# Kernel optimization log

Hardware: AMD Instinct MI355X
Metric: run time of the kernel (lower is better)

## Reference

```python
import jax, jax.numpy as jnp
import numpy as np


def setup_inputs() -> dict:
    key = jax.random.key(0)
    k1, k2 = jax.random.split(key)
    B, N, M = 4, 16384, 4096
    src_points = jax.random.normal(k1, (B, N, 3), dtype=jnp.float32)
    target_verts = jax.random.normal(k2, (B, M, 3), dtype=jnp.float32)
    return {"src_points": src_points, "target_verts": target_verts}


def reference(src_points, target_verts):
    # target_faces=None path of ChamferLoss: degenerate one-vertex triangles,
    # so closest-point-on-mesh == nearest target vertex.
    # d2[b,n,m] = ||p_bn - v_bm||^2 via the expansion p2 + v2 - 2 p.v
    p2 = jnp.sum(src_points * src_points, axis=-1)          # (B, N)
    v2 = jnp.sum(target_verts * target_verts, axis=-1)      # (B, M)
    pv = jnp.einsum('bnd,bmd->bnm', src_points, target_verts)  # (B, N, M)
    d2 = p2[:, :, None] + v2[:, None, :] - 2.0 * pv
    d2 = jnp.maximum(d2, 0.0)
    min_d2 = jnp.min(d2, axis=-1)                            # (B, N)
    num_src_per_batch = src_points.shape[1]
    loss = jnp.sum(min_d2, axis=-1) / num_src_per_batch      # (B,)
    return loss
```

## Files before the change

kernel.cpp:

```cpp
#include <hip/hip_runtime.h>
#include <float.h>


typedef __bf16 bf16x8 __attribute__((ext_vector_type(8)));
typedef float  f32x16 __attribute__((ext_vector_type(16)));

constexpr int B = 4, N = 16384, M = 4096;
constexpr int BN = B * N;
constexpr int VT = 8;
constexpr int NVC = M / (VT * 32);
constexpr int G = 4;
constexpr int TPB = 256;
constexpr int PPB = 4 * G * 32;
constexpr int NPB = BN / PPB;

constexpr size_t VFRAG_BYTES = (size_t)B * M * 32;
constexpr size_t PFRAG_BYTES = (size_t)BN * 32;
constexpr size_t PP_BYTES    = (size_t)BN * 4;

__global__ __launch_bounds__(256) void chamfer_pre(
    const float* __restrict__ src, const float* __restrict__ tv,
    unsigned char* __restrict__ vfr, unsigned char* __restrict__ pfr,
    float* __restrict__ pp, float* __restrict__ out)
{
    if (blockIdx.x == 0 && threadIdx.x < B) out[threadIdx.x] = 0.0f;
    __bf16 one = (__bf16)1.0f, zero = (__bf16)0.0f;

    if (blockIdx.x < (B * M) / 256) {
        int i = blockIdx.x * 256 + threadIdx.x;
        float x = tv[3 * i + 0], y = tv[3 * i + 1], z = tv[3 * i + 2];
        __bf16 xh = (__bf16)x, yh = (__bf16)y, zh = (__bf16)z;
        float xhf = (float)xh, yhf = (float)yh, zhf = (float)zh;
        __bf16 xl = (__bf16)(x - xhf), yl = (__bf16)(y - yhf), zl = (__bf16)(z - zhf);
        float v2 = fmaf(x, x, fmaf(y, y, z * z));
        __bf16 v2h = (__bf16)v2;
        __bf16 v2l = (__bf16)(v2 - (float)v2h);

        bf16x8 h0, h1;
        h0[0] = (__bf16)(-2.0f * xhf); h0[1] = (__bf16)(-2.0f * yhf);
        h0[2] = (__bf16)(-2.0f * zhf);
        h0[3] = h0[0]; h0[4] = h0[1]; h0[5] = h0[2];
        h0[6] = (__bf16)(-2.0f * (float)xl); h0[7] = (__bf16)(-2.0f * (float)yl);
        h1[0] = (__bf16)(-2.0f * (float)zl); h1[1] = v2h; h1[2] = v2l;
        h1[3] = zero; h1[4] = zero; h1[5] = zero; h1[6] = zero; h1[7] = zero;

        int m = i & (M - 1);
        size_t base = (size_t)(i >> 12) * 131072 + (size_t)(m >> 5) * 1024
                    + (size_t)(m & 31) * 16;
        *(bf16x8*)(vfr + base)       = h0;
        *(bf16x8*)(vfr + base + 512) = h1;
    } else {
        int i = (blockIdx.x - (B * M) / 256) * 256 + threadIdx.x;
        float x = src[3 * i + 0], y = src[3 * i + 1], z = src[3 * i + 2];
        __bf16 xh = (__bf16)x, yh = (__bf16)y, zh = (__bf16)z;
        __bf16 xl = (__bf16)(x - (float)xh), yl = (__bf16)(y - (float)yh),
               zl = (__bf16)(z - (float)zh);
        bf16x8 h0, h1;
        h0[0] = xh; h0[1] = yh; h0[2] = zh; h0[3] = xl;
        h0[4] = yl; h0[5] = zl; h0[6] = xh; h0[7] = yh;
        h1[0] = zh; h1[1] = one; h1[2] = one; h1[3] = zero;
        h1[4] = zero; h1[5] = zero; h1[6] = zero; h1[7] = zero;

        size_t base = (size_t)(i >> 5) * 1024 + (size_t)(i & 31) * 16;
        *(bf16x8*)(pfr + base)       = h0;
        *(bf16x8*)(pfr + base + 512) = h1;
        pp[i] = fmaf(x, x, fmaf(y, y, z * z));
    }
}

__global__ __launch_bounds__(TPB) void chamfer_mfma(
    const unsigned char* __restrict__ vfr, const unsigned char* __restrict__ pfr,
    float* __restrict__ partial)
{
    const int blk  = blockIdx.x;
    const int vc   = blk & (NVC - 1);
    const int pblk = blk >> 4;
    const int b    = pblk >> 5;
    const int t    = threadIdx.x;
    const int w    = t >> 6, L = t & 63;
    const int half = L >> 5, c = L & 31;
    const int laneoff = half * 512 + c * 16;

    const unsigned char* abase =
        vfr + (size_t)b * 131072 + (size_t)vc * (VT * 1024) + laneoff;
    bf16x8 av[VT];
#pragma unroll
    for (int tt = 0; tt < VT; ++tt)
        av[tt] = *(const bf16x8*)(abase + tt * 1024);

    const int pg0 = pblk * (PPB / 32) + w * G;
    bf16x8 bP[G];
#pragma unroll
    for (int g = 0; g < G; ++g)
        bP[g] = *(const bf16x8*)(pfr + (size_t)(pg0 + g) * 1024 + laneoff);

    f32x16 zeroC;
#pragma unroll
    for (int r = 0; r < 16; ++r) zeroC[r] = 0.0f;

#pragma unroll
    for (int g = 0; g < G; ++g) {
        float mn[8];
#pragma unroll
        for (int u = 0; u < 8; ++u) mn[u] = FLT_MAX;
#pragma unroll
        for (int tt = 0; tt < VT; ++tt) {
            f32x16 C = __builtin_amdgcn_mfma_f32_32x32x16_bf16(
                av[tt], bP[g], zeroC, 0, 0, 0);
#pragma unroll
            for (int u = 0; u < 8; ++u)
                mn[u] = fminf(fminf(mn[u], C[2 * u]), C[2 * u + 1]);
        }
        float m01 = fminf(fminf(mn[0], mn[1]), fminf(mn[2], mn[3]));
        float m23 = fminf(fminf(mn[4], mn[5]), fminf(mn[6], mn[7]));
        float m = fminf(m01, m23);
        m = fminf(m, __shfl_xor(m, 32, 64));
        if (L < 32)
            partial[(size_t)vc * BN + (size_t)(pg0 + g) * 32 + c] = m;
    }
}

__global__ __launch_bounds__(256) void chamfer_reduce(
    const float* __restrict__ partial, const float* __restrict__ pp,
    float* __restrict__ out)
{
    const int p = blockIdx.x * 256 + threadIdx.x;
    const int b = blockIdx.x >> 6;
    float m = FLT_MAX;
#pragma unroll
    for (int vc = 0; vc < NVC; ++vc)
        m = fminf(m, partial[(size_t)vc * BN + p]);
    float sum = fmaxf(m + pp[p], 0.0f);

    for (int off = 32; off > 0; off >>= 1)
        sum += __shfl_down(sum, off, 64);
    __shared__ float acc[4];
    if ((threadIdx.x & 63) == 0) acc[threadIdx.x >> 6] = sum;
    __syncthreads();
    if (threadIdx.x == 0) {
        float s = acc[0] + acc[1] + acc[2] + acc[3];
        atomicAdd(&out[b], s * (1.0f / N));
    }
}

extern "C" void kernel_launch(void* const* d_in, const int* in_sizes, int n_in,
                              void* d_out, int out_size, void* d_ws, size_t ws_size,
                              hipStream_t stream) {
    const float* src = (const float*)d_in[0];
    const float* tv  = (const float*)d_in[1];
    float* out = (float*)d_out;

    unsigned char* vfr = (unsigned char*)d_ws;
    unsigned char* pfr = vfr + VFRAG_BYTES;
    float* pp          = (float*)(pfr + PFRAG_BYTES);
    float* partial     = (float*)((char*)pp + PP_BYTES);

    chamfer_pre   <<<(B * M) / 256 + BN / 256, 256, 0, stream>>>(src, tv, vfr, pfr, pp, out);
    chamfer_mfma  <<<NVC * NPB, TPB, 0, stream>>>(vfr, pfr, partial);
    chamfer_reduce<<<BN / 256, 256, 0, stream>>>(partial, pp, out);
}
```

Before: 77.73 us.

## Fuse point prep and min-reduction into one MFMA kernel over all vertices

The point-fragment preprocessing and the separate reduce kernel are removed. Each 512-thread block now builds its bf16 point fragments in registers from the raw source points. Two wave groups each sweep half of the vertex tiles, and the block combines the two halves through LDS before the atomic batch sum. This drops the partial-minimum buffer round trip, a kernel launch and the pfr/pp workspace traffic. In exchange the grid shrinks to 256 blocks with vertex fragments streamed each iteration instead of preloaded, so there is less occupancy and latency hiding.

```diff
diff --git a/kernel.cpp b/kernel.cpp
--- a/kernel.cpp
+++ b/kernel.cpp
@@ -7,139 +7,129 @@
 
 constexpr int B = 4, N = 16384, M = 4096;
 constexpr int BN = B * N;
-constexpr int VT = 8;
-constexpr int NVC = M / (VT * 32);
-constexpr int G = 4;
-constexpr int TPB = 256;
-constexpr int PPB = 4 * G * 32;
+constexpr int TILES = M / 32;
+constexpr int HT = TILES / 2;
+constexpr int TPB = 512;
+constexpr int PPB = 256;
 constexpr int NPB = BN / PPB;
 
 constexpr size_t VFRAG_BYTES = (size_t)B * M * 32;
-constexpr size_t PFRAG_BYTES = (size_t)BN * 32;
-constexpr size_t PP_BYTES    = (size_t)BN * 4;
 
 __global__ __launch_bounds__(256) void chamfer_pre(
-    const float* __restrict__ src, const float* __restrict__ tv,
-    unsigned char* __restrict__ vfr, unsigned char* __restrict__ pfr,
-    float* __restrict__ pp, float* __restrict__ out)
+    const float* __restrict__ tv, unsigned char* __restrict__ vfr,
+    float* __restrict__ out)
 {
     if (blockIdx.x == 0 && threadIdx.x < B) out[threadIdx.x] = 0.0f;
-    __bf16 one = (__bf16)1.0f, zero = (__bf16)0.0f;
+    int i = blockIdx.x * 256 + threadIdx.x;
+    float x = tv[3 * i + 0], y = tv[3 * i + 1], z = tv[3 * i + 2];
+    __bf16 xh = (__bf16)x, yh = (__bf16)y, zh = (__bf16)z;
+    float xhf = (float)xh, yhf = (float)yh, zhf = (float)zh;
+    __bf16 xl = (__bf16)(x - xhf), yl = (__bf16)(y - yhf), zl = (__bf16)(z - zhf);
+    float v2 = fmaf(x, x, fmaf(y, y, z * z));
+    __bf16 v2h = (__bf16)v2;
+    __bf16 v2l = (__bf16)(v2 - (float)v2h);
+    __bf16 zero = (__bf16)0.0f;
 
-    if (blockIdx.x < (B * M) / 256) {
-        int i = blockIdx.x * 256 + threadIdx.x;
-        float x = tv[3 * i + 0], y = tv[3 * i + 1], z = tv[3 * i + 2];
-        __bf16 xh = (__bf16)x, yh = (__bf16)y, zh = (__bf16)z;
-        float xhf = (float)xh, yhf = (float)yh, zhf = (float)zh;
-        __bf16 xl = (__bf16)(x - xhf), yl = (__bf16)(y - yhf), zl = (__bf16)(z - zhf);
-        float v2 = fmaf(x, x, fmaf(y, y, z * z));
-        __bf16 v2h = (__bf16)v2;
-        __bf16 v2l = (__bf16)(v2 - (float)v2h);
+    bf16x8 h0, h1;
+    h0[0] = (__bf16)(-2.0f * xhf); h0[1] = (__bf16)(-2.0f * yhf);
+    h0[2] = (__bf16)(-2.0f * zhf);
+    h0[3] = h0[0]; h0[4] = h0[1]; h0[5] = h0[2];
+    h0[6] = (__bf16)(-2.0f * (float)xl); h0[7] = (__bf16)(-2.0f * (float)yl);
+    h1[0] = (__bf16)(-2.0f * (float)zl); h1[1] = v2h; h1[2] = v2l;
+    h1[3] = zero; h1[4] = zero; h1[5] = zero; h1[6] = zero; h1[7] = zero;
 
-        bf16x8 h0, h1;
-        h0[0] = (__bf16)(-2.0f * xhf); h0[1] = (__bf16)(-2.0f * yhf);
-        h0[2] = (__bf16)(-2.0f * zhf);
-        h0[3] = h0[0]; h0[4] = h0[1]; h0[5] = h0[2];
-        h0[6] = (__bf16)(-2.0f * (float)xl); h0[7] = (__bf16)(-2.0f * (float)yl);
-        h1[0] = (__bf16)(-2.0f * (float)zl); h1[1] = v2h; h1[2] = v2l;
-        h1[3] = zero; h1[4] = zero; h1[5] = zero; h1[6] = zero; h1[7] = zero;
-
-        int m = i & (M - 1);
-        size_t base = (size_t)(i >> 12) * 131072 + (size_t)(m >> 5) * 1024
-                    + (size_t)(m & 31) * 16;
-        *(bf16x8*)(vfr + base)       = h0;
-        *(bf16x8*)(vfr + base + 512) = h1;
-    } else {
-        int i = (blockIdx.x - (B * M) / 256) * 256 + threadIdx.x;
-        float x = src[3 * i + 0], y = src[3 * i + 1], z = src[3 * i + 2];
-        __bf16 xh = (__bf16)x, yh = (__bf16)y, zh = (__bf16)z;
-        __bf16 xl = (__bf16)(x - (float)xh), yl = (__bf16)(y - (float)yh),
-               zl = (__bf16)(z - (float)zh);
-        bf16x8 h0, h1;
-        h0[0] = xh; h0[1] = yh; h0[2] = zh; h0[3] = xl;
-        h0[4] = yl; h0[5] = zl; h0[6] = xh; h0[7] = yh;
-        h1[0] = zh; h1[1] = one; h1[2] = one; h1[3] = zero;
-        h1[4] = zero; h1[5] = zero; h1[6] = zero; h1[7] = zero;
-
-        size_t base = (size_t)(i >> 5) * 1024 + (size_t)(i & 31) * 16;
-        *(bf16x8*)(pfr + base)       = h0;
-        *(bf16x8*)(pfr + base + 512) = h1;
-        pp[i] = fmaf(x, x, fmaf(y, y, z * z));
-    }
+    int m = i & (M - 1);
+    size_t base = (size_t)(i >> 12) * 131072 + (size_t)(m >> 5) * 1024
+                + (size_t)(m & 31) * 16;
+    *(bf16x8*)(vfr + base)       = h0;
+    *(bf16x8*)(vfr + base + 512) = h1;
 }
 
-__global__ __launch_bounds__(TPB) void chamfer_mfma(
-    const unsigned char* __restrict__ vfr, const unsigned char* __restrict__ pfr,
-    float* __restrict__ partial)
+__global__ __launch_bounds__(TPB) void chamfer_main(
+    const float* __restrict__ src, const unsigned char* __restrict__ vfr,
+    float* __restrict__ out)
 {
-    const int blk  = blockIdx.x;
-    const int vc   = blk & (NVC - 1);
-    const int pblk = blk >> 4;
-    const int b    = pblk >> 5;
+    const int pblk = blockIdx.x;
+    const int b    = pblk >> 6;
     const int t    = threadIdx.x;
     const int w    = t >> 6, L = t & 63;
+    const int s    = w & 3, h = w >> 2;
     const int half = L >> 5, c = L & 31;
     const int laneoff = half * 512 + c * 16;
 
-    const unsigned char* abase =
-        vfr + (size_t)b * 131072 + (size_t)vc * (VT * 1024) + laneoff;
-    bf16x8 av[VT];
-#pragma unroll
-    for (int tt = 0; tt < VT; ++tt)
-        av[tt] = *(const bf16x8*)(abase + tt * 1024);
+    const int P0 = pblk * PPB + s * 64;
+    const int p0 = P0 + c, p1 = P0 + 32 + c;
+    float x0 = src[3 * p0], y0 = src[3 * p0 + 1], z0 = src[3 * p0 + 2];
+    float x1 = src[3 * p1], y1 = src[3 * p1 + 1], z1 = src[3 * p1 + 2];
+    float pp0 = fmaf(x0, x0, fmaf(y0, y0, z0 * z0));
+    float pp1 = fmaf(x1, x1, fmaf(y1, y1, z1 * z1));
 
-    const int pg0 = pblk * (PPB / 32) + w * G;
-    bf16x8 bP[G];
-#pragma unroll
-    for (int g = 0; g < G; ++g)
-        bP[g] = *(const bf16x8*)(pfr + (size_t)(pg0 + g) * 1024 + laneoff);
+    __bf16 one = (__bf16)1.0f, zero = (__bf16)0.0f;
+    bf16x8 bP0, bP1;
+    {
+        __bf16 xh = (__bf16)x0, yh = (__bf16)y0, zh = (__bf16)z0;
+        __bf16 xl = (__bf16)(x0 - (float)xh), yl = (__bf16)(y0 - (float)yh),
+               zl = (__bf16)(z0 - (float)zh);
+        if (half == 0) { bP0[0]=xh; bP0[1]=yh; bP0[2]=zh; bP0[3]=xl; bP0[4]=yl; bP0[5]=zl; bP0[6]=xh; bP0[7]=yh; }
+        else { bP0[0]=zh; bP0[1]=one; bP0[2]=one; bP0[3]=zero; bP0[4]=zero; bP0[5]=zero; bP0[6]=zero; bP0[7]=zero; }
+    }
+    {
+        __bf16 xh = (__bf16)x1, yh = (__bf16)y1, zh = (__bf16)z1;
+        __bf16 xl = (__bf16)(x1 - (float)xh), yl = (__bf16)(y1 - (float)yh),
+               zl = (__bf16)(z1 - (float)zh);
+        if (half == 0) { bP1[0]=xh; bP1[1]=yh; bP1[2]=zh; bP1[3]=xl; bP1[4]=yl; bP1[5]=zl; bP1[6]=xh; bP1[7]=yh; }
+        else { bP1[0]=zh; bP1[1]=one; bP1[2]=one; bP1[3]=zero; bP1[4]=zero; bP1[5]=zero; bP1[6]=zero; bP1[7]=zero; }
+    }
 
     f32x16 zeroC;
 #pragma unroll
     for (int r = 0; r < 16; ++r) zeroC[r] = 0.0f;
+    float mn0[8], mn1[8];
+#pragma unroll
+    for (int u = 0; u < 8; ++u) { mn0[u] = FLT_MAX; mn1[u] = FLT_MAX; }
 
+    const unsigned char* abase =
+        vfr + (size_t)b * 131072 + (size_t)h * (HT * 1024) + laneoff;
+#pragma unroll 8
+    for (int tt = 0; tt < HT; ++tt) {
+        bf16x8 av = *(const bf16x8*)(abase + tt * 1024);
+        f32x16 C0 = __builtin_amdgcn_mfma_f32_32x32x16_bf16(av, bP0, zeroC, 0, 0, 0);
+        f32x16 C1 = __builtin_amdgcn_mfma_f32_32x32x16_bf16(av, bP1, zeroC, 0, 0, 0);
 #pragma unroll
-    for (int g = 0; g < G; ++g) {
-        float mn[8];
-#pragma unroll
-        for (int u = 0; u < 8; ++u) mn[u] = FLT_MAX;
-#pragma unroll
-        for (int tt = 0; tt < VT; ++tt) {
-            f32x16 C = __builtin_amdgcn_mfma_f32_32x32x16_bf16(
-                av[tt], bP[g], zeroC, 0, 0, 0);
-#pragma unroll
-            for (int u = 0; u < 8; ++u)
-                mn[u] = fminf(fminf(mn[u], C[2 * u]), C[2 * u + 1]);
+        for (int u = 0; u < 8; ++u) {
+            mn0[u] = fminf(fminf(mn0[u], C0[2 * u]), C0[2 * u + 1]);
+            mn1[u] = fminf(fminf(mn1[u], C1[2 * u]), C1[2 * u + 1]);
         }
-        float m01 = fminf(fminf(mn[0], mn[1]), fminf(mn[2], mn[3]));
-        float m23 = fminf(fminf(mn[4], mn[5]), fminf(mn[6], mn[7]));
-        float m = fminf(m01, m23);
-        m = fminf(m, __shfl_xor(m, 32, 64));
-        if (L < 32)
-            partial[(size_t)vc * BN + (size_t)(pg0 + g) * 32 + c] = m;
     }
-}
 
-__global__ __launch_bounds__(256) void chamfer_reduce(
-    const float* __restrict__ partial, const float* __restrict__ pp,
-    float* __restrict__ out)
-{
-    const int p = blockIdx.x * 256 + threadIdx.x;
-    const int b = blockIdx.x >> 6;
-    float m = FLT_MAX;
-#pragma unroll
-    for (int vc = 0; vc < NVC; ++vc)
-        m = fminf(m, partial[(size_t)vc * BN + p]);
-    float sum = fmaxf(m + pp[p], 0.0f);
+    float a01 = fminf(fminf(mn0[0], mn0[1]), fminf(mn0[2], mn0[3]));
+    float a23 = fminf(fminf(mn0[4], mn0[5]), fminf(mn0[6], mn0[7]));
+    float m0 = fminf(a01, a23);
+    m0 = fminf(m0, __shfl_xor(m0, 32, 64));
+    float b01 = fminf(fminf(mn1[0], mn1[1]), fminf(mn1[2], mn1[3]));
+    float b23 = fminf(fminf(mn1[4], mn1[5]), fminf(mn1[6], mn1[7]));
+    float m1 = fminf(b01, b23);
+    m1 = fminf(m1, __shfl_xor(m1, 32, 64));
+    float m  = half ? m1 : m0;
+    float pp = half ? pp1 : pp0;
 
+    __shared__ float lds_m[TPB];
+    __shared__ float acc[8];
+    lds_m[t] = m;
+    __syncthreads();
+
+    float sum = 0.0f;
+    if (w < 4) {
+        float mm = fminf(m, lds_m[t + 256]);
+        sum = fmaxf(mm + pp, 0.0f);
+    }
     for (int off = 32; off > 0; off >>= 1)
         sum += __shfl_down(sum, off, 64);
-    __shared__ float acc[4];
-    if ((threadIdx.x & 63) == 0) acc[threadIdx.x >> 6] = sum;
+    if (L == 0) acc[w] = sum;
     __syncthreads();
-    if (threadIdx.x == 0) {
-        float s = acc[0] + acc[1] + acc[2] + acc[3];
-        atomicAdd(&out[b], s * (1.0f / N));
+    if (t == 0) {
+        float ssum = acc[0] + acc[1] + acc[2] + acc[3];
+        atomicAdd(&out[b], ssum * (1.0f / N));
     }
 }
 
@@ -149,13 +139,8 @@
     const float* src = (const float*)d_in[0];
     const float* tv  = (const float*)d_in[1];
     float* out = (float*)d_out;
+    unsigned char* vfr = (unsigned char*)d_ws;
 
-    unsigned char* vfr = (unsigned char*)d_ws;
-    unsigned char* pfr = vfr + VFRAG_BYTES;
-    float* pp          = (float*)(pfr + PFRAG_BYTES);
-    float* partial     = (float*)((char*)pp + PP_BYTES);
-
-    chamfer_pre   <<<(B * M) / 256 + BN / 256, 256, 0, stream>>>(src, tv, vfr, pfr, pp, out);
-    chamfer_mfma  <<<NVC * NPB, TPB, 0, stream>>>(vfr, pfr, partial);
-    chamfer_reduce<<<BN / 256, 256, 0, stream>>>(partial, pp, out);
+    chamfer_pre <<<(B * M) / 256, 256, 0, stream>>>(tv, vfr, out);
+    chamfer_main<<<NPB, TPB, 0, stream>>>(src, vfr, out);
 }
```

Result: faster. 69.49 us (-10.6%).
